# Kernel tuning notes

Hardware: AMD Instinct MI355X
Metric: run time of the kernel (lower is better)

Reference implementation:

```python
import jax, jax.numpy as jnp
import numpy as np

B, S, E, H = 2, 2048, 1024, 16
D = E // H
LN_EPS = 1e-5
NORM_EPS = 1e-12  # F.normalize clamp_min


def setup_inputs() -> dict:
    key = jax.random.key(0)
    ks = jax.random.split(key, 4)
    x = jax.random.normal(ks[0], (B, S, E), dtype=jnp.float32)
    qkv_w = jax.random.normal(ks[1], (3 * E, E), dtype=jnp.float32) * 0.02
    qkv_b = jnp.zeros((3 * E,), dtype=jnp.float32)
    out_w = jax.random.normal(ks[2], (E, E), dtype=jnp.float32) * 0.02
    out_b = jnp.zeros((E,), dtype=jnp.float32)
    ln_w = jnp.ones((E,), dtype=jnp.float32)
    ln_b = jnp.zeros((E,), dtype=jnp.float32)
    qknorm_scale = jnp.asarray(E ** -0.5, dtype=jnp.float32)
    # RotaryEmbedding buffer: inv_freq interleaved (emb[::2] = emb[1::2] = base**(-arange(0,E,2)/E))
    base_freq = 10000.0 ** (-(np.arange(0, E, 2).astype(np.float32) / E))
    emb = np.empty((E,), dtype=np.float32)
    emb[::2] = base_freq
    emb[1::2] = base_freq
    inv_freq = jnp.asarray(emb)
    return {"x": x, "ln_w": ln_w, "ln_b": ln_b, "qkv_w": qkv_w, "qkv_b": qkv_b,
            "qknorm_scale": qknorm_scale, "out_w": out_w, "out_b": out_b, "inv_freq": inv_freq}


def _rotate(t, sin, cos):
    # Faithful to source: x1 = even idx (excluding last), x2 = odd idx; cat(-x2, x1)
    x1 = t[..., :-1:2]
    x2 = t[..., 1::2]
    t_rot = jnp.concatenate((-x2, x1), axis=-1)
    return t * cos + t_rot * sin


def _l2norm(t):
    n = jnp.sqrt(jnp.sum(t * t, axis=-1, keepdims=True))
    return t / jnp.maximum(n, NORM_EPS)


def reference(x, ln_w, ln_b, qkv_w, qkv_b, qknorm_scale, out_w, out_b, inv_freq):
    # --- prenorm (LayerNorm, eps=1e-5) ---
    mu = jnp.mean(x, axis=-1, keepdims=True)
    var = jnp.mean((x - mu) ** 2, axis=-1, keepdims=True)
    xn = (x - mu) / jnp.sqrt(var + LN_EPS) * ln_w + ln_b
    # --- QKV projection ---
    qkv = xn @ qkv_w.T + qkv_b  # [B,S,3E]
    q, k, v = jnp.split(qkv, 3, axis=-1)
    # --- rotary (source uses scalar seq*inv_freq, not per-position) ---
    seq = q.shape[1]
    sin = jnp.sin(seq * inv_freq)
    cos = jnp.cos(seq * inv_freq)
    q = _rotate(q, sin, cos)
    k = _rotate(k, sin, cos)
    # --- split heads: [B,S,E] -> [B,H,S,D] ---
    split = lambda t: t.reshape(B, seq, H, D).transpose(0, 2, 1, 3)
    q, k, v = split(q), split(k), split(v)
    # --- qknorm ---
    q = _l2norm(q) * qknorm_scale
    k = _l2norm(k) * qknorm_scale
    # --- scaled dot product with causal mask ---
    aw = jnp.einsum('bhqd,bhkd->bhqk', q, k)  # [B,H,S,S]
    causal = jnp.tril(jnp.ones((seq, seq), dtype=bool))
    aw = jnp.where(causal, aw, jnp.finfo(aw.dtype).min)
    aw = jax.nn.softmax(aw, axis=-1)
    attn = jnp.einsum('bhqk,bhkd->bhqd', aw, v)
    # --- merge heads + out proj ---
    attn = attn.transpose(0, 2, 1, 3).reshape(B, seq, E)
    return attn @ out_w.T + out_b
```

## Files before the change

kernel.cpp:

```cpp
#include <hip/hip_runtime.h>

typedef unsigned short u16;
typedef __attribute__((ext_vector_type(8))) short bf16x8;
typedef __attribute__((ext_vector_type(4))) float f32x4;

#define SS 2048
#define EE 1024
#define HH 16
#define DD 64

__device__ __forceinline__ float b2f(u16 u) {
  union { unsigned int i; float f; } v; v.i = ((unsigned int)u) << 16; return v.f;
}
__device__ __forceinline__ u16 f2b(float f) {
  union { float f; unsigned int i; } v; v.f = f;
  unsigned int i = v.i;
  return (u16)((i + 0x7FFFu + ((i >> 16) & 1u)) >> 16);
}
__device__ __forceinline__ unsigned int cvt_pk_bf16(float lo, float hi) {
  unsigned int r;
  asm("v_cvt_pk_bf16_f32 %0, %1, %2" : "=v"(r) : "v"(lo), "v"(hi));
  return r;
}

#define GLD16(g, l)                                                         \
  __builtin_amdgcn_global_load_lds(                                         \
      (const __attribute__((address_space(1))) unsigned int*)(g),           \
      (__attribute__((address_space(3))) unsigned int*)(l), 16, 0, 0)

__global__ __launch_bounds__(256) void k_prep(const float* __restrict__ qkv_w,
                                              u16* __restrict__ wq_b,
                                              const float* __restrict__ inv_freq,
                                              float2* __restrict__ cs,
                                              const float* __restrict__ x,
                                              const float* __restrict__ lw,
                                              const float* __restrict__ lb,
                                              u16* __restrict__ xn) {
  const int bx = blockIdx.x, t = threadIdx.x;
  if (bx < 3072) {
    const int i = bx * 256 + t;
    float4 v = ((const float4*)qkv_w)[i];
    ushort4 o;
    o.x = f2b(v.x); o.y = f2b(v.y); o.z = f2b(v.z); o.w = f2b(v.w);
    ((ushort4*)wq_b)[i] = o;
    return;
  }
  if (bx < 3076) {
    const int i = (bx - 3072) * 256 + t;
    float th = 2048.0f * inv_freq[i];
    cs[i] = make_float2(cosf(th), sinf(th));
    return;
  }
  const int row = bx - 3076;
  float4 v = ((const float4*)(x + (size_t)row * EE))[t];
  float f0 = v.x, f1 = v.y, f2 = v.z, f3 = v.w;
  float s = f0 + f1 + f2 + f3;
  float ss = f0 * f0 + f1 * f1 + f2 * f2 + f3 * f3;
  for (int o = 1; o < 64; o <<= 1) { s += __shfl_xor(s, o); ss += __shfl_xor(ss, o); }
  __shared__ float red[8];
  int w = t >> 6;
  if ((t & 63) == 0) { red[w] = s; red[4 + w] = ss; }
  __syncthreads();
  s = red[0] + red[1] + red[2] + red[3];
  ss = red[4] + red[5] + red[6] + red[7];
  float mu = s * (1.0f / 1024.0f);
  float var = ss * (1.0f / 1024.0f) - mu * mu;
  float rstd = rsqrtf(var + 1e-5f);
  float4 wv = ((const float4*)lw)[t];
  float4 bv = ((const float4*)lb)[t];
  ushort4 o;
  o.x = f2b((f0 - mu) * rstd * wv.x + bv.x);
  o.y = f2b((f1 - mu) * rstd * wv.y + bv.y);
  o.z = f2b((f2 - mu) * rstd * wv.z + bv.z);
  o.w = f2b((f3 - mu) * rstd * wv.w + bv.w);
  ((ushort4*)(xn + (size_t)row * EE))[t] = o;
}

__global__ __launch_bounds__(256) void k_gemm_b(const u16* __restrict__ A,
                                                const u16* __restrict__ W,
                                                const float* __restrict__ bias,
                                                u16* __restrict__ C,
                                                u16* __restrict__ VT,
                                                int M, int N, int K) {
  __shared__ __align__(16) u16 As[128 * 32];
  __shared__ __align__(16) u16 Ws[128 * 32];
  __shared__ __align__(16) u16 Tt[128 * 136];
  const int t = threadIdx.x;
  const int m0 = blockIdx.y * 128, n0 = blockIdx.x * 128;
  const int lane = t & 63, w = t >> 6, quad = lane >> 4, l15 = lane & 15;
  const int wm = (w & 1) * 64, wn = (w >> 1) * 64;

  f32x4 zero4 = {0.f, 0.f, 0.f, 0.f};
  f32x4 acc[4][4];
  for (int mi = 0; mi < 4; mi++)
    for (int ni = 0; ni < 4; ni++) acc[mi][ni] = zero4;

  const u16* Ag = A + (size_t)(m0 + (t >> 2)) * K + (t & 3) * 8;
  const u16* Wg = W + (size_t)(n0 + (t >> 2)) * K + (t & 3) * 8;
  const size_t rowskip = (size_t)64 * K;

  for (int k0 = 0; k0 < K; k0 += 32) {
    GLD16(Ag + k0, As + t * 8);
    GLD16(Ag + rowskip + k0, As + 2048 + t * 8);
    GLD16(Wg + k0, Ws + t * 8);
    GLD16(Wg + rowskip + k0, Ws + 2048 + t * 8);
    __syncthreads();
    bf16x8 af[4], wf[4];
#pragma unroll
    for (int i = 0; i < 4; i++) {
      af[i] = *(const bf16x8*)(As + (wm + i * 16 + l15) * 32 + quad * 8);
      wf[i] = *(const bf16x8*)(Ws + (wn + i * 16 + l15) * 32 + quad * 8);
    }
#pragma unroll
    for (int mi = 0; mi < 4; mi++)
#pragma unroll
      for (int ni = 0; ni < 4; ni++)
        acc[mi][ni] = __builtin_amdgcn_mfma_f32_16x16x32_bf16(af[mi], wf[ni], acc[mi][ni], 0, 0, 0);
    __syncthreads();
  }
  if (n0 < 2048) {
    for (int mi = 0; mi < 4; mi++)
      for (int ni = 0; ni < 4; ni++) {
        int col = n0 + wn + ni * 16 + l15;
        float bb = bias[col];
        for (int r = 0; r < 4; r++) {
          int grow = m0 + wm + mi * 16 + quad * 4 + r;
          C[(size_t)grow * N + col] = f2b(acc[mi][ni][r] + bb);
        }
      }
  } else {
    for (int mi = 0; mi < 4; mi++)
      for (int ni = 0; ni < 4; ni++) {
        int cn = wn + ni * 16 + l15;
        int sIn = wm + mi * 16 + quad * 4;
        float bb = bias[n0 + cn];
        ushort4 o;
        o.x = f2b(acc[mi][ni][0] + bb);
        o.y = f2b(acc[mi][ni][1] + bb);
        o.z = f2b(acc[mi][ni][2] + bb);
        o.w = f2b(acc[mi][ni][3] + bb);
        *(ushort4*)(Tt + cn * 136 + sIn) = o;
      }
    __syncthreads();
    const int cn = t >> 1, half = t & 1;
    const int h = (n0 - 2048 + cn) >> 6, d = cn & 63;
    const int bb_ = m0 >> 11, s0 = (m0 & 2047) + half * 64;
    u16* dst = VT + ((size_t)((bb_ * 16 + h) * 64 + d)) * SS + s0;
    const u16* srcT = Tt + cn * 136 + half * 64;
#pragma unroll
    for (int it = 0; it < 8; it++)
      *(bf16x8*)(dst + it * 8) = *(const bf16x8*)(srcT + it * 8);
  }
}

__global__ __launch_bounds__(256) void k_gemm_fw(const u16* __restrict__ A,
                                                 const float* __restrict__ W,
                                                 const float* __restrict__ bias,
                                                 float* __restrict__ C,
                                                 int M, int N, int K) {
  __shared__ __align__(16) u16 As[64 * 32];
  __shared__ __align__(16) u16 Ws[128 * 32];
  const int t = threadIdx.x;
  const int m0 = blockIdx.y * 64, n0 = blockIdx.x * 128;
  const int lane = t & 63, w = t >> 6, quad = lane >> 4, l15 = lane & 15;
  const int wm = (w & 1) * 32, wn = (w >> 1) * 64;

  f32x4 zero4 = {0.f, 0.f, 0.f, 0.f};
  f32x4 acc[2][4];
  for (int mi = 0; mi < 2; mi++)
    for (int ni = 0; ni < 4; ni++) acc[mi][ni] = zero4;

  const u16* Ag = A + (size_t)(m0 + (t >> 2)) * K + (t & 3) * 8;
  const float* Wg0 = W + (size_t)(n0 + (t >> 2)) * K + (t & 3) * 8;
  const float* Wg1 = Wg0 + (size_t)64 * K;

  for (int k0 = 0; k0 < K; k0 += 32) {
    GLD16(Ag + k0, As + t * 8);
    float4 wa = *(const float4*)(Wg0 + k0);
    float4 wb = *(const float4*)(Wg0 + k0 + 4);
    float4 wc = *(const float4*)(Wg1 + k0);
    float4 wd = *(const float4*)(Wg1 + k0 + 4);
    union { unsigned int u[4]; bf16x8 v8; } p0, p1;
    p0.u[0] = cvt_pk_bf16(wa.x, wa.y); p0.u[1] = cvt_pk_bf16(wa.z, wa.w);
    p0.u[2] = cvt_pk_bf16(wb.x, wb.y); p0.u[3] = cvt_pk_bf16(wb.z, wb.w);
    p1.u[0] = cvt_pk_bf16(wc.x, wc.y); p1.u[1] = cvt_pk_bf16(wc.z, wc.w);
    p1.u[2] = cvt_pk_bf16(wd.x, wd.y); p1.u[3] = cvt_pk_bf16(wd.z, wd.w);
    *(bf16x8*)(Ws + t * 8) = p0.v8;
    *(bf16x8*)(Ws + 2048 + t * 8) = p1.v8;
    __syncthreads();
    bf16x8 af[2], wf[4];
#pragma unroll
    for (int i = 0; i < 2; i++)
      af[i] = *(const bf16x8*)(As + (wm + i * 16 + l15) * 32 + quad * 8);
#pragma unroll
    for (int i = 0; i < 4; i++)
      wf[i] = *(const bf16x8*)(Ws + (wn + i * 16 + l15) * 32 + quad * 8);
#pragma unroll
    for (int mi = 0; mi < 2; mi++)
#pragma unroll
      for (int ni = 0; ni < 4; ni++)
        acc[mi][ni] = __builtin_amdgcn_mfma_f32_16x16x32_bf16(af[mi], wf[ni], acc[mi][ni], 0, 0, 0);
    __syncthreads();
  }
  for (int mi = 0; mi < 2; mi++)
    for (int ni = 0; ni < 4; ni++) {
      int col = n0 + wn + ni * 16 + l15;
      float bb = bias[col];
      for (int r = 0; r < 4; r++) {
        int grow = m0 + wm + mi * 16 + quad * 4 + r;
        C[(size_t)grow * N + col] = acc[mi][ni][r] + bb;
      }
    }
}

__global__ __launch_bounds__(256) void k_rotv(u16* __restrict__ qkv,
                                              const float2* __restrict__ cs_tab,
                                              const float* __restrict__ scale_p) {
  __shared__ float qf[1024];
  __shared__ float kf[1024];
  const int row = blockIdx.x, t = threadIdx.x;
  u16* qr = qkv + (size_t)row * 3072;
  u16* kr = qr + 1024;
  ushort4 qv = ((const ushort4*)qr)[t];
  ushort4 kv = ((const ushort4*)kr)[t];
  *(float4*)(qf + 4 * t) = make_float4(b2f(qv.x), b2f(qv.y), b2f(qv.z), b2f(qv.w));
  *(float4*)(kf + 4 * t) = make_float4(b2f(kv.x), b2f(kv.y), b2f(kv.z), b2f(kv.w));
  __syncthreads();
  const float scale = scale_p[0];
  float rq[4], rk[4];
#pragma unroll
  for (int u = 0; u < 4; u++) {
    int j = 4 * t + u;
    float2 cs = cs_tab[j];
    float qrot = (j < 512) ? -qf[2 * j + 1] : qf[2 * (j - 512)];
    float krot = (j < 512) ? -kf[2 * j + 1] : kf[2 * (j - 512)];
    rq[u] = qf[j] * cs.x + qrot * cs.y;
    rk[u] = kf[j] * cs.x + krot * cs.y;
  }
  float ssq = rq[0] * rq[0] + rq[1] * rq[1] + rq[2] * rq[2] + rq[3] * rq[3];
  float ssk = rk[0] * rk[0] + rk[1] * rk[1] + rk[2] * rk[2] + rk[3] * rk[3];
  for (int o = 1; o < 16; o <<= 1) { ssq += __shfl_xor(ssq, o); ssk += __shfl_xor(ssk, o); }
  float qs = scale / fmaxf(sqrtf(ssq), 1e-12f);
  float ks = scale / fmaxf(sqrtf(ssk), 1e-12f);
  ushort4 qo, ko;
  qo.x = f2b(rq[0] * qs); qo.y = f2b(rq[1] * qs); qo.z = f2b(rq[2] * qs); qo.w = f2b(rq[3] * qs);
  ko.x = f2b(rk[0] * ks); ko.y = f2b(rk[1] * ks); ko.z = f2b(rk[2] * ks); ko.w = f2b(rk[3] * ks);
  ((ushort4*)qr)[t] = qo;
  ((ushort4*)kr)[t] = ko;
}

__global__ __launch_bounds__(512, 4) void k_attn(const u16* __restrict__ qkv,
                                                 const u16* __restrict__ vt,
                                                 u16* __restrict__ out) {
  __shared__ __align__(16) u16 Kt[2][128 * 72];
  __shared__ __align__(16) u16 Vt[2][64 * 136];
  const int bh = blockIdx.x;
  const int y = blockIdx.y;
  const int qt = (y < 8) ? y : 23 - y;
  const int b = bh >> 4, h = bh & 15;
  const int t = threadIdx.x, w = t >> 6, lane = t & 63, quad = lane >> 4, l15 = lane & 15;
  const int krow = t >> 2, kq = (t & 3) * 16;
  const int dr = t >> 3, kc8 = t & 7;
  const int srcl = (lane & 48) + ((lane >> 4) << 2);
  const int qA = ((lane >> 4) & 1) * 32 + l15;
  const int qB = qA + 16;
  const bool hiN = (quad >> 1) & 1;
  const u16* kn = qkv + 1024;
  f32x4 zero4 = {0.f, 0.f, 0.f, 0.f};
  const int q0 = qt * 128;

  bf16x8 qf[2];
  {
    const u16* qrow = qkv + (size_t)(b * SS + q0 + 16 * w + l15) * 3072 + h * DD;
    qf[0] = *(const bf16x8*)(qrow + quad * 8);
    qf[1] = *(const bf16x8*)(qrow + 32 + quad * 8);
  }
  f32x4 oacc[4];
  for (int n = 0; n < 4; n++) oacc[n] = zero4;
  float m_i = -1e30f, l_i = 0.f;

  bf16x8 kv[2], vv[2];
  {
    const u16* krg = kn + (size_t)(b * SS + krow) * 3072 + h * DD + kq;
    kv[0] = *(const bf16x8*)(krg);
    kv[1] = *(const bf16x8*)(krg + 8);
    const u16* vrg = vt + (size_t)(bh * DD + dr) * SS + kc8 * 16;
    vv[0] = *(const bf16x8*)(vrg);
    vv[1] = *(const bf16x8*)(vrg + 8);
  }
  *(bf16x8*)(Kt[0] + krow * 72 + kq) = kv[0];
  *(bf16x8*)(Kt[0] + krow * 72 + kq + 8) = kv[1];
  *(bf16x8*)(Vt[0] + dr * 136 + kc8 * 16) = vv[0];
  *(bf16x8*)(Vt[0] + dr * 136 + kc8 * 16 + 8) = vv[1];
  __syncthreads();
  int cur = 0;

  for (int kt = 0; kt <= qt; kt++) {
    if (kt < qt) {
      const int k0n = (kt + 1) * 128;
      const u16* krg = kn + (size_t)(b * SS + k0n + krow) * 3072 + h * DD + kq;
      kv[0] = *(const bf16x8*)(krg);
      kv[1] = *(const bf16x8*)(krg + 8);
      const u16* vrg = vt + (size_t)(bh * DD + dr) * SS + k0n + kc8 * 16;
      vv[0] = *(const bf16x8*)(vrg);
      vv[1] = *(const bf16x8*)(vrg + 8);
    }
    const u16* Kc = Kt[cur];
    const u16* Vc = Vt[cur];
    f32x4 sacc[8];
    __builtin_amdgcn_s_setprio(1);
#pragma unroll
    for (int n = 0; n < 8; n++) {
      sacc[n] = zero4;
#pragma unroll
      for (int c = 0; c < 2; c++) {
        bf16x8 kfrag = *(const bf16x8*)(Kc + (n * 16 + l15) * 72 + c * 32 + quad * 8);
        sacc[n] = __builtin_amdgcn_mfma_f32_16x16x32_bf16(kfrag, qf[c], sacc[n], 0, 0, 0);
      }
    }
    __builtin_amdgcn_s_setprio(0);
    if (kt == qt) {
      const int qrow = 16 * w + l15, kbase = 4 * quad;
#pragma unroll
      for (int n = 0; n < 8; n++)
#pragma unroll
        for (int r = 0; r < 4; r++)
          if (16 * n + kbase + r > qrow) sacc[n][r] = -1e30f;
    }
    float mx = -1e30f;
#pragma unroll
    for (int n = 0; n < 8; n++)
#pragma unroll
      for (int r = 0; r < 4; r++) mx = fmaxf(mx, sacc[n][r]);
    mx = fmaxf(mx, __shfl_xor(mx, 16));
    mx = fmaxf(mx, __shfl_xor(mx, 32));
    const bool need = !__all(mx - m_i <= 8.0f);
    float al = 1.0f;
    if (need) {
      float mn = fmaxf(m_i, mx);
      al = __expf(m_i - mn);
      m_i = mn;
    }
    float rs = 0.f;
#pragma unroll
    for (int n = 0; n < 8; n++)
#pragma unroll
      for (int r = 0; r < 4; r++) {
        float p = __expf(sacc[n][r] - m_i);
        sacc[n][r] = p;
        rs += p;
      }
    rs += __shfl_xor(rs, 16);
    rs += __shfl_xor(rs, 32);
    l_i = al * l_i + rs;
    if (need) {
      float alr[4];
#pragma unroll
      for (int r = 0; r < 4; r++) alr[r] = __shfl(al, srcl + r);
#pragma unroll
      for (int n = 0; n < 4; n++)
#pragma unroll
        for (int r = 0; r < 4; r++) oacc[n][r] *= alr[r];
    }
    unsigned int pkw[8][2];
#pragma unroll
    for (int n = 0; n < 8; n++) {
      pkw[n][0] = cvt_pk_bf16(sacc[n][0], sacc[n][1]);
      pkw[n][1] = cvt_pk_bf16(sacc[n][2], sacc[n][3]);
    }
#pragma unroll
    for (int c = 0; c < 4; c++) {
      unsigned int a0 = __shfl(pkw[2 * c][0], qA);
      unsigned int a1 = __shfl(pkw[2 * c][1], qA);
      unsigned int a2 = __shfl(pkw[2 * c][0], qB);
      unsigned int a3 = __shfl(pkw[2 * c][1], qB);
      unsigned int b0 = __shfl(pkw[2 * c + 1][0], qA);
      unsigned int b1 = __shfl(pkw[2 * c + 1][1], qA);
      unsigned int b2 = __shfl(pkw[2 * c + 1][0], qB);
      unsigned int b3 = __shfl(pkw[2 * c + 1][1], qB);
      union { unsigned int u[4]; bf16x8 v8; } pf;
      pf.u[0] = hiN ? b0 : a0;
      pf.u[1] = hiN ? b1 : a1;
      pf.u[2] = hiN ? b2 : a2;
      pf.u[3] = hiN ? b3 : a3;
      __builtin_amdgcn_s_setprio(1);
#pragma unroll
      for (int n = 0; n < 4; n++) {
        bf16x8 vf = *(const bf16x8*)(Vc + (n * 16 + l15) * 136 + c * 32 + quad * 8);
        oacc[n] = __builtin_amdgcn_mfma_f32_16x16x32_bf16(pf.v8, vf, oacc[n], 0, 0, 0);
      }
      __builtin_amdgcn_s_setprio(0);
    }
    if (kt < qt) {
      *(bf16x8*)(Kt[cur ^ 1] + krow * 72 + kq) = kv[0];
      *(bf16x8*)(Kt[cur ^ 1] + krow * 72 + kq + 8) = kv[1];
      *(bf16x8*)(Vt[cur ^ 1] + dr * 136 + kc8 * 16) = vv[0];
      *(bf16x8*)(Vt[cur ^ 1] + dr * 136 + kc8 * 16 + 8) = vv[1];
    }
    __syncthreads();
    cur ^= 1;
  }
  float lr[4];
#pragma unroll
  for (int r = 0; r < 4; r++) lr[r] = __shfl(l_i, srcl + r);
  for (int n = 0; n < 4; n++)
    for (int r = 0; r < 4; r++) {
      int row = q0 + 16 * w + quad * 4 + r;
      out[(size_t)(b * SS + row) * EE + h * DD + n * 16 + l15] = f2b(oacc[n][r] / lr[r]);
    }
}

extern "C" void kernel_launch(void* const* d_in, const int* in_sizes, int n_in,
                              void* d_out, int out_size, void* d_ws, size_t ws_size,
                              hipStream_t stream) {
  const float* x       = (const float*)d_in[0];
  const float* ln_w    = (const float*)d_in[1];
  const float* ln_b    = (const float*)d_in[2];
  const float* qkv_w   = (const float*)d_in[3];
  const float* qkv_b   = (const float*)d_in[4];
  const float* qk_s    = (const float*)d_in[5];
  const float* out_w   = (const float*)d_in[6];
  const float* out_b   = (const float*)d_in[7];
  const float* inv_frq = (const float*)d_in[8];

  u16* ws   = (u16*)d_ws;
  u16* xn   = ws;
  u16* qkv  = ws + (size_t)4096 * 1024;
  u16* wq_b = (u16*)d_out;
  float2* cs_tab = (float2*)((char*)d_out + 6291456);
  u16* vt   = (u16*)d_out + (size_t)4194304;

  k_prep<<<7172, 256, 0, stream>>>(qkv_w, wq_b, inv_frq, cs_tab, x, ln_w, ln_b, xn);
  k_gemm_b<<<dim3(24, 32), 256, 0, stream>>>(xn, wq_b, qkv_b, qkv, vt, 4096, 3072, 1024);
  k_rotv<<<4096, 256, 0, stream>>>(qkv, cs_tab, qk_s);
  k_attn<<<dim3(32, 16), 512, 0, stream>>>(qkv, vt, xn);
  k_gemm_fw<<<dim3(8, 64), 256, 0, stream>>>(xn, out_w, out_b, (float*)d_out, 4096, 1024, 1024);
}
```

Measured before the change: 233.6 us.

## Double-buffer GEMM LDS tiles, shrink V transpose buffer, drop attention lazy rescale and setprio

Both GEMM kernels now double-buffer their shared-memory A and W tiles, prefetching the next K-slice during the current MFMA step and removing one barrier per iteration. The QKV GEMM's V-transpose staging buffer is halved and written in two passes, which keeps LDS use near its old size. The attention kernel drops the conditional lazy rescaling and always rescales the accumulator, and it removes the s_setprio hints. The last two attention edits look like reverts of earlier tweaks and may add per-tile work, while the extra LDS in the GEMMs could reduce occupancy.

```diff
diff --git a/kernel.cpp b/kernel.cpp
--- a/kernel.cpp
+++ b/kernel.cpp
@@ -82,9 +82,9 @@
                                                 u16* __restrict__ C,
                                                 u16* __restrict__ VT,
                                                 int M, int N, int K) {
-  __shared__ __align__(16) u16 As[128 * 32];
-  __shared__ __align__(16) u16 Ws[128 * 32];
-  __shared__ __align__(16) u16 Tt[128 * 136];
+  __shared__ __align__(16) u16 As[2][128 * 32];
+  __shared__ __align__(16) u16 Ws[2][128 * 32];
+  __shared__ __align__(16) u16 Tt[64 * 136];
   const int t = threadIdx.x;
   const int m0 = blockIdx.y * 128, n0 = blockIdx.x * 128;
   const int lane = t & 63, w = t >> 6, quad = lane >> 4, l15 = lane & 15;
@@ -99,17 +99,25 @@
   const u16* Wg = W + (size_t)(n0 + (t >> 2)) * K + (t & 3) * 8;
   const size_t rowskip = (size_t)64 * K;
 
+  GLD16(Ag, As[0] + t * 8);
+  GLD16(Ag + rowskip, As[0] + 2048 + t * 8);
+  GLD16(Wg, Ws[0] + t * 8);
+  GLD16(Wg + rowskip, Ws[0] + 2048 + t * 8);
+  __syncthreads();
+  int cur = 0;
+
   for (int k0 = 0; k0 < K; k0 += 32) {
-    GLD16(Ag + k0, As + t * 8);
-    GLD16(Ag + rowskip + k0, As + 2048 + t * 8);
-    GLD16(Wg + k0, Ws + t * 8);
-    GLD16(Wg + rowskip + k0, Ws + 2048 + t * 8);
-    __syncthreads();
+    if (k0 + 32 < K) {
+      GLD16(Ag + k0 + 32, As[cur ^ 1] + t * 8);
+      GLD16(Ag + rowskip + k0 + 32, As[cur ^ 1] + 2048 + t * 8);
+      GLD16(Wg + k0 + 32, Ws[cur ^ 1] + t * 8);
+      GLD16(Wg + rowskip + k0 + 32, Ws[cur ^ 1] + 2048 + t * 8);
+    }
     bf16x8 af[4], wf[4];
 #pragma unroll
     for (int i = 0; i < 4; i++) {
-      af[i] = *(const bf16x8*)(As + (wm + i * 16 + l15) * 32 + quad * 8);
-      wf[i] = *(const bf16x8*)(Ws + (wn + i * 16 + l15) * 32 + quad * 8);
+      af[i] = *(const bf16x8*)(As[cur] + (wm + i * 16 + l15) * 32 + quad * 8);
+      wf[i] = *(const bf16x8*)(Ws[cur] + (wn + i * 16 + l15) * 32 + quad * 8);
     }
 #pragma unroll
     for (int mi = 0; mi < 4; mi++)
@@ -117,7 +125,9 @@
       for (int ni = 0; ni < 4; ni++)
         acc[mi][ni] = __builtin_amdgcn_mfma_f32_16x16x32_bf16(af[mi], wf[ni], acc[mi][ni], 0, 0, 0);
     __syncthreads();
-  }
+    cur ^= 1;
+  }
+
   if (n0 < 2048) {
     for (int mi = 0; mi < 4; mi++)
       for (int ni = 0; ni < 4; ni++) {
@@ -129,27 +139,36 @@
         }
       }
   } else {
-    for (int mi = 0; mi < 4; mi++)
-      for (int ni = 0; ni < 4; ni++) {
-        int cn = wn + ni * 16 + l15;
-        int sIn = wm + mi * 16 + quad * 4;
-        float bb = bias[n0 + cn];
-        ushort4 o;
-        o.x = f2b(acc[mi][ni][0] + bb);
-        o.y = f2b(acc[mi][ni][1] + bb);
-        o.z = f2b(acc[mi][ni][2] + bb);
-        o.w = f2b(acc[mi][ni][3] + bb);
-        *(ushort4*)(Tt + cn * 136 + sIn) = o;
-      }
-    __syncthreads();
-    const int cn = t >> 1, half = t & 1;
-    const int h = (n0 - 2048 + cn) >> 6, d = cn & 63;
-    const int bb_ = m0 >> 11, s0 = (m0 & 2047) + half * 64;
-    u16* dst = VT + ((size_t)((bb_ * 16 + h) * 64 + d)) * SS + s0;
-    const u16* srcT = Tt + cn * 136 + half * 64;
-#pragma unroll
-    for (int it = 0; it < 8; it++)
-      *(bf16x8*)(dst + it * 8) = *(const bf16x8*)(srcT + it * 8);
+#pragma unroll
+    for (int p = 0; p < 2; p++) {
+      if (wn == p * 64) {
+        for (int mi = 0; mi < 4; mi++)
+          for (int ni = 0; ni < 4; ni++) {
+            int cl = ni * 16 + l15;
+            int sIn = wm + mi * 16 + quad * 4;
+            float bb = bias[n0 + p * 64 + cl];
+            ushort4 o;
+            o.x = f2b(acc[mi][ni][0] + bb);
+            o.y = f2b(acc[mi][ni][1] + bb);
+            o.z = f2b(acc[mi][ni][2] + bb);
+            o.w = f2b(acc[mi][ni][3] + bb);
+            *(ushort4*)(Tt + cl * 136 + sIn) = o;
+          }
+      }
+      __syncthreads();
+      {
+        int cl = t >> 2, seg = t & 3;
+        int col = (n0 - 2048) + p * 64 + cl;
+        int h = col >> 6, d = col & 63;
+        int bb_ = m0 >> 11, s0 = (m0 & 2047) + seg * 32;
+        u16* dst = VT + ((size_t)((bb_ * 16 + h) * 64 + d)) * SS + s0;
+        const u16* srcT = Tt + cl * 136 + seg * 32;
+#pragma unroll
+        for (int it = 0; it < 4; it++)
+          *(bf16x8*)(dst + it * 8) = *(const bf16x8*)(srcT + it * 8);
+      }
+      if (p == 0) __syncthreads();
+    }
   }
 }
 
@@ -158,8 +177,8 @@
                                                  const float* __restrict__ bias,
                                                  float* __restrict__ C,
                                                  int M, int N, int K) {
-  __shared__ __align__(16) u16 As[64 * 32];
-  __shared__ __align__(16) u16 Ws[128 * 32];
+  __shared__ __align__(16) u16 As[2][64 * 32];
+  __shared__ __align__(16) u16 Ws[2][128 * 32];
   const int t = threadIdx.x;
   const int m0 = blockIdx.y * 64, n0 = blockIdx.x * 128;
   const int lane = t & 63, w = t >> 6, quad = lane >> 4, l15 = lane & 15;
@@ -174,33 +193,55 @@
   const float* Wg0 = W + (size_t)(n0 + (t >> 2)) * K + (t & 3) * 8;
   const float* Wg1 = Wg0 + (size_t)64 * K;
 
-  for (int k0 = 0; k0 < K; k0 += 32) {
-    GLD16(Ag + k0, As + t * 8);
-    float4 wa = *(const float4*)(Wg0 + k0);
-    float4 wb = *(const float4*)(Wg0 + k0 + 4);
-    float4 wc = *(const float4*)(Wg1 + k0);
-    float4 wd = *(const float4*)(Wg1 + k0 + 4);
+  float4 wa = *(const float4*)(Wg0);
+  float4 wb = *(const float4*)(Wg0 + 4);
+  float4 wc = *(const float4*)(Wg1);
+  float4 wd = *(const float4*)(Wg1 + 4);
+  GLD16(Ag, As[0] + t * 8);
+  {
     union { unsigned int u[4]; bf16x8 v8; } p0, p1;
     p0.u[0] = cvt_pk_bf16(wa.x, wa.y); p0.u[1] = cvt_pk_bf16(wa.z, wa.w);
     p0.u[2] = cvt_pk_bf16(wb.x, wb.y); p0.u[3] = cvt_pk_bf16(wb.z, wb.w);
     p1.u[0] = cvt_pk_bf16(wc.x, wc.y); p1.u[1] = cvt_pk_bf16(wc.z, wc.w);
     p1.u[2] = cvt_pk_bf16(wd.x, wd.y); p1.u[3] = cvt_pk_bf16(wd.z, wd.w);
-    *(bf16x8*)(Ws + t * 8) = p0.v8;
-    *(bf16x8*)(Ws + 2048 + t * 8) = p1.v8;
-    __syncthreads();
+    *(bf16x8*)(Ws[0] + t * 8) = p0.v8;
+    *(bf16x8*)(Ws[0] + 2048 + t * 8) = p1.v8;
+  }
+  __syncthreads();
+  int cur = 0;
+
+  for (int k0 = 0; k0 < K; k0 += 32) {
+    const bool pref = (k0 + 32 < K);
+    if (pref) {
+      GLD16(Ag + k0 + 32, As[cur ^ 1] + t * 8);
+      wa = *(const float4*)(Wg0 + k0 + 32);
+      wb = *(const float4*)(Wg0 + k0 + 36);
+      wc = *(const float4*)(Wg1 + k0 + 32);
+      wd = *(const float4*)(Wg1 + k0 + 36);
+    }
     bf16x8 af[2], wf[4];
 #pragma unroll
     for (int i = 0; i < 2; i++)
-      af[i] = *(const bf16x8*)(As + (wm + i * 16 + l15) * 32 + quad * 8);
+      af[i] = *(const bf16x8*)(As[cur] + (wm + i * 16 + l15) * 32 + quad * 8);
 #pragma unroll
     for (int i = 0; i < 4; i++)
-      wf[i] = *(const bf16x8*)(Ws + (wn + i * 16 + l15) * 32 + quad * 8);
+      wf[i] = *(const bf16x8*)(Ws[cur] + (wn + i * 16 + l15) * 32 + quad * 8);
 #pragma unroll
     for (int mi = 0; mi < 2; mi++)
 #pragma unroll
       for (int ni = 0; ni < 4; ni++)
         acc[mi][ni] = __builtin_amdgcn_mfma_f32_16x16x32_bf16(af[mi], wf[ni], acc[mi][ni], 0, 0, 0);
+    if (pref) {
+      union { unsigned int u[4]; bf16x8 v8; } p0, p1;
+      p0.u[0] = cvt_pk_bf16(wa.x, wa.y); p0.u[1] = cvt_pk_bf16(wa.z, wa.w);
+      p0.u[2] = cvt_pk_bf16(wb.x, wb.y); p0.u[3] = cvt_pk_bf16(wb.z, wb.w);
+      p1.u[0] = cvt_pk_bf16(wc.x, wc.y); p1.u[1] = cvt_pk_bf16(wc.z, wc.w);
+      p1.u[2] = cvt_pk_bf16(wd.x, wd.y); p1.u[3] = cvt_pk_bf16(wd.z, wd.w);
+      *(bf16x8*)(Ws[cur ^ 1] + t * 8) = p0.v8;
+      *(bf16x8*)(Ws[cur ^ 1] + 2048 + t * 8) = p1.v8;
+    }
     __syncthreads();
+    cur ^= 1;
   }
   for (int mi = 0; mi < 2; mi++)
     for (int ni = 0; ni < 4; ni++) {
@@ -308,7 +349,6 @@
     const u16* Kc = Kt[cur];
     const u16* Vc = Vt[cur];
     f32x4 sacc[8];
-    __builtin_amdgcn_s_setprio(1);
 #pragma unroll
     for (int n = 0; n < 8; n++) {
       sacc[n] = zero4;
@@ -318,7 +358,6 @@
         sacc[n] = __builtin_amdgcn_mfma_f32_16x16x32_bf16(kfrag, qf[c], sacc[n], 0, 0, 0);
       }
     }
-    __builtin_amdgcn_s_setprio(0);
     if (kt == qt) {
       const int qrow = 16 * w + l15, kbase = 4 * quad;
 #pragma unroll
@@ -334,34 +373,28 @@
       for (int r = 0; r < 4; r++) mx = fmaxf(mx, sacc[n][r]);
     mx = fmaxf(mx, __shfl_xor(mx, 16));
     mx = fmaxf(mx, __shfl_xor(mx, 32));
-    const bool need = !__all(mx - m_i <= 8.0f);
-    float al = 1.0f;
-    if (need) {
-      float mn = fmaxf(m_i, mx);
-      al = __expf(m_i - mn);
-      m_i = mn;
-    }
+    float mn = fmaxf(m_i, mx);
+    float al = __expf(m_i - mn);
+    m_i = mn;
     float rs = 0.f;
 #pragma unroll
     for (int n = 0; n < 8; n++)
 #pragma unroll
       for (int r = 0; r < 4; r++) {
-        float p = __expf(sacc[n][r] - m_i);
+        float p = __expf(sacc[n][r] - mn);
         sacc[n][r] = p;
         rs += p;
       }
     rs += __shfl_xor(rs, 16);
     rs += __shfl_xor(rs, 32);
     l_i = al * l_i + rs;
-    if (need) {
-      float alr[4];
-#pragma unroll
-      for (int r = 0; r < 4; r++) alr[r] = __shfl(al, srcl + r);
-#pragma unroll
-      for (int n = 0; n < 4; n++)
-#pragma unroll
-        for (int r = 0; r < 4; r++) oacc[n][r] *= alr[r];
-    }
+    float alr[4];
+#pragma unroll
+    for (int r = 0; r < 4; r++) alr[r] = __shfl(al, srcl + r);
+#pragma unroll
+    for (int n = 0; n < 4; n++)
+#pragma unroll
+      for (int r = 0; r < 4; r++) oacc[n][r] *= alr[r];
     unsigned int pkw[8][2];
 #pragma unroll
     for (int n = 0; n < 8; n++) {
@@ -383,13 +416,11 @@
       pf.u[1] = hiN ? b1 : a1;
       pf.u[2] = hiN ? b2 : a2;
       pf.u[3] = hiN ? b3 : a3;
-      __builtin_amdgcn_s_setprio(1);
 #pragma unroll
       for (int n = 0; n < 4; n++) {
         bf16x8 vf = *(const bf16x8*)(Vc + (n * 16 + l15) * 136 + c * 32 + quad * 8);
         oacc[n] = __builtin_amdgcn_mfma_f32_16x16x32_bf16(pf.v8, vf, oacc[n], 0, 0, 0);
       }
-      __builtin_amdgcn_s_setprio(0);
     }
     if (kt < qt) {
       *(bf16x8*)(Kt[cur ^ 1] + krow * 72 + kq) = kv[0];
```

Measured after the change: 229.1 us. No clear change (-1.9%).
